# Performance work log

Hardware: AMD Instinct MI355X
Metric: run time of the kernel (lower is better)

The kernel has to match this reference:

```python
import jax, jax.numpy as jnp
import numpy as np

D_MODEL = 768
N_HEADS = 12
HEAD_DIM = D_MODEL // N_HEADS


def setup_inputs() -> dict:
    key = jax.random.key(0)
    ks = jax.random.split(key, 9)
    B, S = 2, 2048
    x = jax.random.normal(ks[0], (B, S, D_MODEL), dtype=jnp.float32)
    s = 1.0 / np.sqrt(D_MODEL)
    Wq = jax.random.normal(ks[1], (D_MODEL, D_MODEL), dtype=jnp.float32) * s
    bq = jax.random.normal(ks[2], (D_MODEL,), dtype=jnp.float32) * 0.01
    Wk = jax.random.normal(ks[3], (D_MODEL, D_MODEL), dtype=jnp.float32) * s
    bk = jax.random.normal(ks[4], (D_MODEL,), dtype=jnp.float32) * 0.01
    Wv = jax.random.normal(ks[5], (D_MODEL, D_MODEL), dtype=jnp.float32) * s
    bv = jax.random.normal(ks[6], (D_MODEL,), dtype=jnp.float32) * 0.01
    Wo = jax.random.normal(ks[7], (D_MODEL, D_MODEL), dtype=jnp.float32) * s
    bo = jax.random.normal(ks[8], (D_MODEL,), dtype=jnp.float32) * 0.01
    return {"x": x, "Wq": Wq, "bq": bq, "Wk": Wk, "bk": bk,
            "Wv": Wv, "bv": bv, "Wo": Wo, "bo": bo}


def reference(x, Wq, bq, Wk, bk, Wv, bv, Wo, bo):
    B, S, _ = x.shape
    H, Dh = N_HEADS, HEAD_DIM
    # Projections (torch Linear: x @ W.T + b; here W stored as [in, out])
    q = (x @ Wq + bq).reshape(B, S, H, Dh)
    k = (x @ Wk + bk).reshape(B, S, H, Dh)
    v = (x @ Wv + bv).reshape(B, S, H, Dh)
    scale = 1.0 / jnp.sqrt(jnp.float32(Dh))
    # NOTE: source applies no causal mask despite the class name.
    scores = jnp.einsum('bqhd,bkhd->bhqk', q, k) * scale
    attn = jax.nn.softmax(scores, axis=-1)
    out = jnp.einsum('bhqk,bkhd->bqhd', attn, v).reshape(B, S, H * Dh)
    return out @ Wo + bo
```

## Files before the change

### kernel.cpp

```cpp
#include <hip/hip_runtime.h>

typedef unsigned short u16;
typedef __fp16 halfx2 __attribute__((ext_vector_type(2)));
typedef __fp16 halfx8 __attribute__((ext_vector_type(8)));
typedef float floatx4 __attribute__((ext_vector_type(4)));
typedef unsigned short u16x4 __attribute__((ext_vector_type(4)));
typedef unsigned short u16x8 __attribute__((ext_vector_type(8)));

#define D_MODEL 768
#define NH 12
#define DH 64
#define SEQ 2048
#define BATCH 2
#define MTOK 4096
#define DQKV 2304

__device__ __forceinline__ u16 f2h(float f) {
    __fp16 h = (__fp16)f;
    return __builtin_bit_cast(u16, h);
}

__device__ __forceinline__ void gload_lds16(const void* g, void* l) {
    __builtin_amdgcn_global_load_lds(
        (const __attribute__((address_space(1))) void*)g,
        (__attribute__((address_space(3))) void*)l, 16, 0, 0);
}


__global__ __launch_bounds__(256) void wprep_kernel(const float* __restrict__ Wq, const float* __restrict__ Wk,
                                                    const float* __restrict__ Wv, const float* __restrict__ Wo,
                                                    const float* __restrict__ x,
                                                    u16* __restrict__ WqkvT, u16* __restrict__ WoT,
                                                    u16* __restrict__ xh) {
    __shared__ u16 t[64][72];
    int bid = blockIdx.x;
    int tid = threadIdx.x;
    if (bid >= 576) {
        int idx = (bid - 576) * 2048 + tid * 8;
        float4 v0 = *(const float4*)(x + idx);
        float4 v1 = *(const float4*)(x + idx + 4);
        union { u16x8 u; halfx2 h[4]; } pk;
        pk.h[0] = __builtin_amdgcn_cvt_pkrtz(v0.x, v0.y);
        pk.h[1] = __builtin_amdgcn_cvt_pkrtz(v0.z, v0.w);
        pk.h[2] = __builtin_amdgcn_cvt_pkrtz(v1.x, v1.y);
        pk.h[3] = __builtin_amdgcn_cvt_pkrtz(v1.z, v1.w);
        *(u16x8*)(xh + idx) = pk.u;
        return;
    }
    int z = bid / 144;
    int t2 = bid % 144;
    int k0 = (t2 / 12) * 64, n0 = (t2 % 12) * 64;
    const float* W = (z == 0) ? Wq : (z == 1) ? Wk : (z == 2) ? Wv : Wo;
    u16* dst = (z < 3) ? (WqkvT + (size_t)z * 768 * 768) : WoT;
#pragma unroll
    for (int p = 0; p < 16; ++p) {
        int idx = p * 256 + tid;
        int kr = idx >> 6, nc = idx & 63;
        t[kr][nc] = f2h(W[(size_t)(k0 + kr) * 768 + n0 + nc]);
    }
    __syncthreads();
#pragma unroll
    for (int p = 0; p < 16; ++p) {
        int idx = p * 256 + tid;
        int nr = idx >> 6, kc = idx & 63;
        dst[(size_t)(n0 + nr) * 768 + k0 + kc] = t[kc][nr];
    }
}


__global__ __launch_bounds__(256) void gemm_qkv(const u16* __restrict__ xh, const u16* __restrict__ Bt,
                                                const float* __restrict__ bq, const float* __restrict__ bk,
                                                const float* __restrict__ bv,
                                                u16* __restrict__ qP, u16* __restrict__ kP,
                                                u16* __restrict__ vTout) {
    const int tid = threadIdx.x;
    const int wid = tid >> 6;
    const int lane = tid & 63;
    const int qd = lane >> 4;
    const int l15 = lane & 15;

    const int tn = blockIdx.x * 128;
    const int tm = blockIdx.y * 64;
    const int wm = (wid >> 1) * 32;
    const int wn = (wid & 1) * 64;

    __shared__ alignas(16) u16 As[64 * 64];
    __shared__ alignas(16) u16 Bs[128 * 64];

    floatx4 acc[2][4];
#pragma unroll
    for (int i = 0; i < 2; ++i)
#pragma unroll
        for (int j = 0; j < 4; ++j) acc[i][j] = (floatx4)(0.0f);

    const u16* Ag[2];
#pragma unroll
    for (int rd = 0; rd < 2; ++rd) {
        int s = rd * 256 + tid;
        int r = s >> 3, bl = (s & 7) ^ (r & 7);
        Ag[rd] = xh + (size_t)(tm + r) * 768 + bl * 8;
    }
    const u16* Bg[4];
#pragma unroll
    for (int rd = 0; rd < 4; ++rd) {
        int s = rd * 256 + tid;
        int r = s >> 3, bl = (s & 7) ^ (r & 7);
        Bg[rd] = Bt + (size_t)(tn + r) * 768 + bl * 8;
    }

    for (int kb = 0; kb < 768; kb += 64) {
        __syncthreads();
#pragma unroll
        for (int rd = 0; rd < 2; ++rd)
            gload_lds16(Ag[rd] + kb, As + (size_t)(rd * 256 + tid) * 8);
#pragma unroll
        for (int rd = 0; rd < 4; ++rd)
            gload_lds16(Bg[rd] + kb, Bs + (size_t)(rd * 256 + tid) * 8);
        __syncthreads();

#pragma unroll
        for (int ks = 0; ks < 2; ++ks) {
            halfx8 af[2], bf[4];
#pragma unroll
            for (int i = 0; i < 2; ++i) {
                int r = wm + i * 16 + l15;
                af[i] = *(const halfx8*)(As + r * 64 + (((ks * 4 + qd) ^ (r & 7)) * 8));
            }
#pragma unroll
            for (int j = 0; j < 4; ++j) {
                int r2 = wn + j * 16 + l15;
                bf[j] = *(const halfx8*)(Bs + r2 * 64 + (((ks * 4 + qd) ^ (r2 & 7)) * 8));
            }
#pragma unroll
            for (int i = 0; i < 2; ++i)
#pragma unroll
                for (int j = 0; j < 4; ++j)
                    acc[i][j] = __builtin_amdgcn_mfma_f32_16x16x32_f16(af[i], bf[j], acc[i][j], 0, 0, 0);
        }
    }

    const float cscale = 0.125f * 1.44269504088896340736f;
    const int rgn = (tn < 768) ? 0 : (tn < 1536) ? 1 : 2;
    const float* bsrc = (rgn == 0) ? bq : (rgn == 1) ? bk : bv;
#pragma unroll
    for (int j = 0; j < 4; ++j) {
        int col = tn + wn + j * 16 + l15;
        int cl = col - rgn * 768;
        float bvv = bsrc[cl];
        int h = cl >> 6, d = cl & 63;
#pragma unroll
        for (int i = 0; i < 2; ++i) {
            int row0 = tm + wm + i * 16 + qd * 4;
            int b = row0 >> 11, s0 = row0 & 2047;
            u16x4 pk;
#pragma unroll
            for (int r = 0; r < 4; ++r) {
                float v = acc[i][j][r] + bvv;
                if (rgn == 0) v *= cscale;
                pk[r] = f2h(v);
            }
            if (rgn == 2) {
                *(u16x4*)(vTout + ((size_t)(b * NH + h) * 64 + d) * SEQ + s0) = pk;
            } else {
                u16* dst = (rgn == 0) ? qP : kP;
#pragma unroll
                for (int r = 0; r < 4; ++r)
                    dst[((size_t)(b * NH + h) * SEQ + s0 + r) * DH + d] = pk[r];
            }
        }
    }
}


__global__ __launch_bounds__(256, 3) void attn_kernel(const u16* __restrict__ qP, const u16* __restrict__ kP,
                                                      const u16* __restrict__ vT, u16* __restrict__ attn) {
    const int tid = threadIdx.x;
    const int wid = tid >> 6;
    const int lane = tid & 63;
    const int qd = lane >> 4;
    const int l15 = lane & 15;

    const int bh = blockIdx.x;
    const int b = bh / NH, h = bh % NH;
    const int q0 = blockIdx.y * 64;

    __shared__ alignas(16) u16 smem[13312];
    u16* qlds = smem;
    u16* ps = smem + 4096 + wid * 2304;

#pragma unroll
    for (int ks = 0; ks < 2; ++ks) {
        halfx8 qv = *(const halfx8*)(qP + (size_t)(bh * SEQ + q0 + wid * 16 + l15) * DH + ks * 32 + qd * 8);
        *(halfx8*)(qlds + (size_t)((ks * 4 + wid) * 64 + lane) * 8) = qv;
    }
    __syncthreads();

    auto AQ = [&](int jn, int ks) -> halfx8 {
        return *(const halfx8*)(qlds + (size_t)((ks * 4 + jn) * 64 + lane) * 8);
    };

    floatx4 o[4][4];
#pragma unroll
    for (int ip = 0; ip < 4; ++ip)
#pragma unroll
        for (int jn = 0; jn < 4; ++jn) o[ip][jn] = (floatx4)(0.0f);
    float lsum[4] = {0.0f, 0.0f, 0.0f, 0.0f};

    const u16* kbase = kP + (size_t)(bh * SEQ + wid * 32 + l15) * DH + qd * 8;
    const u16* vbase = vT + (size_t)(bh * 64 + l15) * SEQ + wid * 32 + qd * 8;

    floatx4 sc[2][4];
    {
        halfx8 ak0[2][2];
#pragma unroll
        for (int mi = 0; mi < 2; ++mi)
#pragma unroll
            for (int ks = 0; ks < 2; ++ks)
                ak0[mi][ks] = *(const halfx8*)(kbase + (size_t)(mi * 16) * DH + ks * 32);
#pragma unroll
        for (int jn = 0; jn < 4; ++jn) {
            halfx8 a0 = AQ(jn, 0), a1 = AQ(jn, 1);
#pragma unroll
            for (int mi = 0; mi < 2; ++mi) {
                floatx4 z = (floatx4)(0.0f);
                z = __builtin_amdgcn_mfma_f32_16x16x32_f16(ak0[mi][0], a0, z, 0, 0, 0);
                sc[mi][jn] = __builtin_amdgcn_mfma_f32_16x16x32_f16(ak0[mi][1], a1, z, 0, 0, 0);
            }
        }
    }

    for (int kt = 0; kt < 16; ++kt) {
        const int kt1 = (kt + 1) & 15;

        halfx8 akn[2][2];
#pragma unroll
        for (int mi = 0; mi < 2; ++mi)
#pragma unroll
            for (int ks = 0; ks < 2; ++ks)
                akn[mi][ks] = *(const halfx8*)(kbase + (size_t)(kt1 * 128 + mi * 16) * DH + ks * 32);
        halfx8 avc[4];
#pragma unroll
        for (int ip = 0; ip < 4; ++ip)
            avc[ip] = *(const halfx8*)(vbase + (size_t)(ip * 16) * SEQ + kt * 128);

#pragma unroll
        for (int mi = 0; mi < 2; ++mi)
#pragma unroll
            for (int jn = 0; jn < 4; ++jn) {
                float p0 = __builtin_amdgcn_exp2f(sc[mi][jn][0]);
                float p1 = __builtin_amdgcn_exp2f(sc[mi][jn][1]);
                float p2 = __builtin_amdgcn_exp2f(sc[mi][jn][2]);
                float p3 = __builtin_amdgcn_exp2f(sc[mi][jn][3]);
                lsum[jn] += (p0 + p1) + (p2 + p3);
                union { u16x4 u; halfx2 h[2]; } pk;
                pk.h[0] = __builtin_amdgcn_cvt_pkrtz(p0, p1);
                pk.h[1] = __builtin_amdgcn_cvt_pkrtz(p2, p3);
                *(u16x4*)(ps + (jn * 16 + l15) * 36 + mi * 16 + qd * 4) = pk.u;
            }

        __builtin_amdgcn_s_setprio(1);
#pragma unroll
        for (int jn = 0; jn < 4; ++jn) {
            halfx8 a0 = AQ(jn, 0), a1 = AQ(jn, 1);
#pragma unroll
            for (int mi = 0; mi < 2; ++mi) {
                floatx4 z = (floatx4)(0.0f);
                z = __builtin_amdgcn_mfma_f32_16x16x32_f16(akn[mi][0], a0, z, 0, 0, 0);
                sc[mi][jn] = __builtin_amdgcn_mfma_f32_16x16x32_f16(akn[mi][1], a1, z, 0, 0, 0);
            }
        }
        __builtin_amdgcn_s_setprio(0);

#pragma unroll
        for (int jn = 0; jn < 4; ++jn) {
            union { halfx8 h8; u16x4 u4[2]; } bpu;
            bpu.u4[0] = *(const u16x4*)(ps + (jn * 16 + l15) * 36 + qd * 8);
            bpu.u4[1] = *(const u16x4*)(ps + (jn * 16 + l15) * 36 + qd * 8 + 4);
            __builtin_amdgcn_s_setprio(1);
#pragma unroll
            for (int ip = 0; ip < 4; ++ip)
                o[ip][jn] = __builtin_amdgcn_mfma_f32_16x16x32_f16(avc[ip], bpu.h8, o[ip][jn], 0, 0, 0);
            __builtin_amdgcn_s_setprio(0);
        }
    }

#pragma unroll
    for (int jn = 0; jn < 4; ++jn) {
        float v = lsum[jn];
        v += __shfl_xor(v, 16, 64);
        v += __shfl_xor(v, 32, 64);
        lsum[jn] = v;
    }

    float* Oacc = (float*)smem;
    float* la = (float*)smem + 4352;

    __syncthreads();
    if (wid == 0) {
#pragma unroll
        for (int jn = 0; jn < 4; ++jn) {
            int q = jn * 16 + l15;
#pragma unroll
            for (int ip = 0; ip < 4; ++ip)
                *(floatx4*)(Oacc + q * 68 + ip * 16 + qd * 4) = o[ip][jn];
            if (qd == 0) la[q] = lsum[jn];
        }
    }
    for (int w = 1; w < 4; ++w) {
        __syncthreads();
        if (wid == w) {
#pragma unroll
            for (int jn = 0; jn < 4; ++jn) {
                int q = jn * 16 + l15;
#pragma unroll
                for (int ip = 0; ip < 4; ++ip) {
                    float* p = Oacc + q * 68 + ip * 16 + qd * 4;
                    *(floatx4*)p = *(floatx4*)p + o[ip][jn];
                }
                if (qd == 0) la[q] += lsum[jn];
            }
        }
    }
    __syncthreads();

    {
        int q = tid >> 2, d0 = (tid & 3) * 16;
        float inv = __builtin_amdgcn_rcpf(la[q]);
        const float* op = Oacc + q * 68 + d0;
        u16x8 pk0, pk1;
#pragma unroll
        for (int r = 0; r < 8; ++r) pk0[r] = f2h(op[r] * inv);
#pragma unroll
        for (int r = 0; r < 8; ++r) pk1[r] = f2h(op[8 + r] * inv);
        u16* dst = attn + (size_t)(b * SEQ + q0 + q) * D_MODEL + h * DH + d0;
        *(u16x8*)dst = pk0;
        *(u16x8*)(dst + 8) = pk1;
    }
}


__global__ __launch_bounds__(256) void gemm_out(const u16* __restrict__ A, const u16* __restrict__ Bt,
                                                const float* __restrict__ bias, float* __restrict__ Cout) {
    const int tid = threadIdx.x;
    const int wid = tid >> 6;
    const int lane = tid & 63;
    const int qd = lane >> 4;
    const int l15 = lane & 15;

    const int tn = blockIdx.x * 64;
    const int tm = blockIdx.y * 64;
    const int wm = (wid >> 1) * 32;
    const int wn = (wid & 1) * 32;

    __shared__ alignas(16) u16 As[64 * 64];
    __shared__ alignas(16) u16 Bs[64 * 64];

    floatx4 acc[2][2];
#pragma unroll
    for (int i = 0; i < 2; ++i)
#pragma unroll
        for (int j = 0; j < 2; ++j) acc[i][j] = (floatx4)(0.0f);

    const u16* Ag[2];
    const u16* Bg[2];
#pragma unroll
    for (int rd = 0; rd < 2; ++rd) {
        int s = rd * 256 + tid;
        int r = s >> 3, bl = (s & 7) ^ (r & 7);
        Ag[rd] = A + (size_t)(tm + r) * 768 + bl * 8;
        Bg[rd] = Bt + (size_t)(tn + r) * 768 + bl * 8;
    }

    for (int kb = 0; kb < 768; kb += 64) {
        __syncthreads();
#pragma unroll
        for (int rd = 0; rd < 2; ++rd) {
            gload_lds16(Ag[rd] + kb, As + (size_t)(rd * 256 + tid) * 8);
            gload_lds16(Bg[rd] + kb, Bs + (size_t)(rd * 256 + tid) * 8);
        }
        __syncthreads();

#pragma unroll
        for (int ks = 0; ks < 2; ++ks) {
            halfx8 af[2], bf[2];
#pragma unroll
            for (int i = 0; i < 2; ++i) {
                int r = wm + i * 16 + l15;
                af[i] = *(const halfx8*)(As + r * 64 + (((ks * 4 + qd) ^ (r & 7)) * 8));
                int r2 = wn + i * 16 + l15;
                bf[i] = *(const halfx8*)(Bs + r2 * 64 + (((ks * 4 + qd) ^ (r2 & 7)) * 8));
            }
#pragma unroll
            for (int i = 0; i < 2; ++i)
#pragma unroll
                for (int j = 0; j < 2; ++j)
                    acc[i][j] = __builtin_amdgcn_mfma_f32_16x16x32_f16(af[i], bf[j], acc[i][j], 0, 0, 0);
        }
    }

#pragma unroll
    for (int j = 0; j < 2; ++j) {
        int col = tn + wn + j * 16 + l15;
        float bv = bias[col];
#pragma unroll
        for (int i = 0; i < 2; ++i) {
            int row0 = tm + wm + i * 16 + qd * 4;
#pragma unroll
            for (int r = 0; r < 4; ++r)
                Cout[(size_t)(row0 + r) * 768 + col] = acc[i][j][r] + bv;
        }
    }
}


extern "C" void kernel_launch(void* const* d_in, const int* in_sizes, int n_in,
                              void* d_out, int out_size, void* d_ws, size_t ws_size,
                              hipStream_t stream) {
    const float* x  = (const float*)d_in[0];
    const float* Wq = (const float*)d_in[1];
    const float* bq = (const float*)d_in[2];
    const float* Wk = (const float*)d_in[3];
    const float* bk = (const float*)d_in[4];
    const float* Wv = (const float*)d_in[5];
    const float* bv = (const float*)d_in[6];
    const float* Wo = (const float*)d_in[7];
    const float* bo = (const float*)d_in[8];

    char* ws = (char*)d_ws;
    size_t off = 0;
    auto take = [&](size_t bytes) -> char* {
        char* p = ws + off;
        off += (bytes + 255) & ~(size_t)255;
        return p;
    };
    u16* WqkvT = (u16*)take((size_t)DQKV * D_MODEL * 2);
    u16* WoT   = (u16*)take((size_t)D_MODEL * D_MODEL * 2);
    u16* qP    = (u16*)take((size_t)MTOK * D_MODEL * 2);
    u16* kP    = (u16*)take((size_t)MTOK * D_MODEL * 2);
    u16* vTb   = (u16*)take((size_t)BATCH * NH * DH * SEQ * 2);
    u16* attn  = (u16*)take((size_t)MTOK * D_MODEL * 2);
    u16* xh = attn;

    wprep_kernel<<<576 + (MTOK * D_MODEL / 2048), 256, 0, stream>>>(Wq, Wk, Wv, Wo, x, WqkvT, WoT, xh);
    gemm_qkv<<<dim3(DQKV / 128, MTOK / 64), 256, 0, stream>>>(xh, WqkvT, bq, bk, bv, qP, kP, vTb);
    attn_kernel<<<dim3(BATCH * NH, SEQ / 64), 256, 0, stream>>>(qP, kP, vTb, attn);
    gemm_out<<<dim3(D_MODEL / 64, MTOK / 64), 256, 0, stream>>>(attn, WoT, bo, (float*)d_out);
}
```

Baseline: 197.5 us.

## Split PV output across waves by head-dim with shared P tile

Each wave now owns 16 head-dim columns of the output instead of a partial sum over its own key slice. P tiles from all waves go into a double-buffered shared array and are read by every wave after a per-iteration barrier. This removes the serialized cross-wave reduction of 64x64 fp32 accumulators at the end and shrinks the output accumulator registers fourfold. Q fragments are also kept in registers instead of reloaded from LDS. The cost is a __syncthreads inside every key-tile iteration and a larger shared P buffer.

New measurement: 185.2 us. 1.07x faster.

```diff
diff --git a/kernel.cpp b/kernel.cpp
--- a/kernel.cpp
+++ b/kernel.cpp
@@ -184,30 +184,22 @@
     const int b = bh / NH, h = bh % NH;
     const int q0 = blockIdx.y * 64;
 
-    __shared__ alignas(16) u16 smem[13312];
-    u16* qlds = smem;
-    u16* ps = smem + 4096 + wid * 2304;
-
-#pragma unroll
-    for (int ks = 0; ks < 2; ++ks) {
-        halfx8 qv = *(const halfx8*)(qP + (size_t)(bh * SEQ + q0 + wid * 16 + l15) * DH + ks * 32 + qd * 8);
-        *(halfx8*)(qlds + (size_t)((ks * 4 + wid) * 64 + lane) * 8) = qv;
-    }
-    __syncthreads();
-
-    auto AQ = [&](int jn, int ks) -> halfx8 {
-        return *(const halfx8*)(qlds + (size_t)((ks * 4 + jn) * 64 + lane) * 8);
-    };
-
-    floatx4 o[4][4];
-#pragma unroll
-    for (int ip = 0; ip < 4; ++ip)
-#pragma unroll
-        for (int jn = 0; jn < 4; ++jn) o[ip][jn] = (floatx4)(0.0f);
+    __shared__ alignas(16) u16 smem[2 * 64 * 136];
+
+    halfx8 aq[4][2];
+#pragma unroll
+    for (int jn = 0; jn < 4; ++jn)
+#pragma unroll
+        for (int ks = 0; ks < 2; ++ks)
+            aq[jn][ks] = *(const halfx8*)(qP + (size_t)(bh * SEQ + q0 + jn * 16 + l15) * DH + ks * 32 + qd * 8);
+
+    floatx4 o[4];
+#pragma unroll
+    for (int jn = 0; jn < 4; ++jn) o[jn] = (floatx4)(0.0f);
     float lsum[4] = {0.0f, 0.0f, 0.0f, 0.0f};
 
     const u16* kbase = kP + (size_t)(bh * SEQ + wid * 32 + l15) * DH + qd * 8;
-    const u16* vbase = vT + (size_t)(bh * 64 + l15) * SEQ + wid * 32 + qd * 8;
+    const u16* vbase = vT + (size_t)(bh * 64 + wid * 16 + l15) * SEQ + qd * 8;
 
     floatx4 sc[2][4];
     {
@@ -219,17 +211,17 @@
                 ak0[mi][ks] = *(const halfx8*)(kbase + (size_t)(mi * 16) * DH + ks * 32);
 #pragma unroll
         for (int jn = 0; jn < 4; ++jn) {
-            halfx8 a0 = AQ(jn, 0), a1 = AQ(jn, 1);
 #pragma unroll
             for (int mi = 0; mi < 2; ++mi) {
                 floatx4 z = (floatx4)(0.0f);
-                z = __builtin_amdgcn_mfma_f32_16x16x32_f16(ak0[mi][0], a0, z, 0, 0, 0);
-                sc[mi][jn] = __builtin_amdgcn_mfma_f32_16x16x32_f16(ak0[mi][1], a1, z, 0, 0, 0);
+                z = __builtin_amdgcn_mfma_f32_16x16x32_f16(ak0[mi][0], aq[jn][0], z, 0, 0, 0);
+                sc[mi][jn] = __builtin_amdgcn_mfma_f32_16x16x32_f16(ak0[mi][1], aq[jn][1], z, 0, 0, 0);
             }
         }
     }
 
     for (int kt = 0; kt < 16; ++kt) {
+        u16* pbuf = smem + (size_t)(kt & 1) * (64 * 136);
         const int kt1 = (kt + 1) & 15;
 
         halfx8 akn[2][2];
@@ -240,8 +232,8 @@
                 akn[mi][ks] = *(const halfx8*)(kbase + (size_t)(kt1 * 128 + mi * 16) * DH + ks * 32);
         halfx8 avc[4];
 #pragma unroll
-        for (int ip = 0; ip < 4; ++ip)
-            avc[ip] = *(const halfx8*)(vbase + (size_t)(ip * 16) * SEQ + kt * 128);
+        for (int ks = 0; ks < 4; ++ks)
+            avc[ks] = *(const halfx8*)(vbase + kt * 128 + ks * 32);
 
 #pragma unroll
         for (int mi = 0; mi < 2; ++mi)
@@ -255,33 +247,33 @@
                 union { u16x4 u; halfx2 h[2]; } pk;
                 pk.h[0] = __builtin_amdgcn_cvt_pkrtz(p0, p1);
                 pk.h[1] = __builtin_amdgcn_cvt_pkrtz(p2, p3);
-                *(u16x4*)(ps + (jn * 16 + l15) * 36 + mi * 16 + qd * 4) = pk.u;
+                *(u16x4*)(pbuf + (jn * 16 + l15) * 136 + wid * 32 + mi * 16 + qd * 4) = pk.u;
             }
 
         __builtin_amdgcn_s_setprio(1);
 #pragma unroll
         for (int jn = 0; jn < 4; ++jn) {
-            halfx8 a0 = AQ(jn, 0), a1 = AQ(jn, 1);
 #pragma unroll
             for (int mi = 0; mi < 2; ++mi) {
                 floatx4 z = (floatx4)(0.0f);
-                z = __builtin_amdgcn_mfma_f32_16x16x32_f16(akn[mi][0], a0, z, 0, 0, 0);
-                sc[mi][jn] = __builtin_amdgcn_mfma_f32_16x16x32_f16(akn[mi][1], a1, z, 0, 0, 0);
+                z = __builtin_amdgcn_mfma_f32_16x16x32_f16(akn[mi][0], aq[jn][0], z, 0, 0, 0);
+                sc[mi][jn] = __builtin_amdgcn_mfma_f32_16x16x32_f16(akn[mi][1], aq[jn][1], z, 0, 0, 0);
             }
         }
         __builtin_amdgcn_s_setprio(0);
 
-#pragma unroll
-        for (int jn = 0; jn < 4; ++jn) {
-            union { halfx8 h8; u16x4 u4[2]; } bpu;
-            bpu.u4[0] = *(const u16x4*)(ps + (jn * 16 + l15) * 36 + qd * 8);
-            bpu.u4[1] = *(const u16x4*)(ps + (jn * 16 + l15) * 36 + qd * 8 + 4);
-            __builtin_amdgcn_s_setprio(1);
-#pragma unroll
-            for (int ip = 0; ip < 4; ++ip)
-                o[ip][jn] = __builtin_amdgcn_mfma_f32_16x16x32_f16(avc[ip], bpu.h8, o[ip][jn], 0, 0, 0);
-            __builtin_amdgcn_s_setprio(0);
-        }
+        __syncthreads();
+
+        __builtin_amdgcn_s_setprio(1);
+#pragma unroll
+        for (int ks = 0; ks < 4; ++ks) {
+#pragma unroll
+            for (int jn = 0; jn < 4; ++jn) {
+                halfx8 bp = *(const halfx8*)(pbuf + (jn * 16 + l15) * 136 + ks * 32 + qd * 8);
+                o[jn] = __builtin_amdgcn_mfma_f32_16x16x32_f16(avc[ks], bp, o[jn], 0, 0, 0);
+            }
+        }
+        __builtin_amdgcn_s_setprio(0);
     }
 
 #pragma unroll
@@ -292,49 +284,24 @@
         lsum[jn] = v;
     }
 
-    float* Oacc = (float*)smem;
-    float* la = (float*)smem + 4352;
-
+    float* la4 = (float*)smem;
+    if (qd == 0) {
+#pragma unroll
+        for (int jn = 0; jn < 4; ++jn)
+            la4[wid * 64 + jn * 16 + l15] = lsum[jn];
+    }
     __syncthreads();
-    if (wid == 0) {
-#pragma unroll
-        for (int jn = 0; jn < 4; ++jn) {
-            int q = jn * 16 + l15;
-#pragma unroll
-            for (int ip = 0; ip < 4; ++ip)
-                *(floatx4*)(Oacc + q * 68 + ip * 16 + qd * 4) = o[ip][jn];
-            if (qd == 0) la[q] = lsum[jn];
-        }
-    }
-    for (int w = 1; w < 4; ++w) {
-        __syncthreads();
-        if (wid == w) {
-#pragma unroll
-            for (int jn = 0; jn < 4; ++jn) {
-                int q = jn * 16 + l15;
-#pragma unroll
-                for (int ip = 0; ip < 4; ++ip) {
-                    float* p = Oacc + q * 68 + ip * 16 + qd * 4;
-                    *(floatx4*)p = *(floatx4*)p + o[ip][jn];
-                }
-                if (qd == 0) la[q] += lsum[jn];
-            }
-        }
-    }
-    __syncthreads();
-
-    {
-        int q = tid >> 2, d0 = (tid & 3) * 16;
-        float inv = __builtin_amdgcn_rcpf(la[q]);
-        const float* op = Oacc + q * 68 + d0;
-        u16x8 pk0, pk1;
-#pragma unroll
-        for (int r = 0; r < 8; ++r) pk0[r] = f2h(op[r] * inv);
-#pragma unroll
-        for (int r = 0; r < 8; ++r) pk1[r] = f2h(op[8 + r] * inv);
-        u16* dst = attn + (size_t)(b * SEQ + q0 + q) * D_MODEL + h * DH + d0;
-        *(u16x8*)dst = pk0;
-        *(u16x8*)(dst + 8) = pk1;
+
+#pragma unroll
+    for (int jn = 0; jn < 4; ++jn) {
+        int q = jn * 16 + l15;
+        float s = (la4[q] + la4[64 + q]) + (la4[128 + q] + la4[192 + q]);
+        float inv = __builtin_amdgcn_rcpf(s);
+        u16x4 pk;
+#pragma unroll
+        for (int r = 0; r < 4; ++r) pk[r] = f2h(o[jn][r] * inv);
+        u16* dst = attn + (size_t)(b * SEQ + q0 + q) * D_MODEL + h * DH + wid * 16 + qd * 4;
+        *(u16x4*)dst = pk;
     }
 }
 
```

## Software-pipeline attention loop with double-buffered P tiles and register-resident Q

Applied to the files above, without the earlier changes.

Restructures the attention main loop into a deeper software pipeline. K tiles are prefetched two iterations ahead, V is double-buffered in registers, and the softmax probability tile is double-buffered in LDS so the QK, exp and PV stages of different iterations overlap. Q fragments are now held in registers instead of being staged through LDS, which removes the initial barrier. The extra register and LDS use lowers the occupancy hint from 3 to 2 blocks per CU, which may reduce latency hiding.

Measured after the change: 206.6 us. 1.05x slower.

```diff
diff --git a/kernel.cpp b/kernel.cpp
--- a/kernel.cpp
+++ b/kernel.cpp
@@ -172,7 +172,7 @@
 }
 
 
-__global__ __launch_bounds__(256, 3) void attn_kernel(const u16* __restrict__ qP, const u16* __restrict__ kP,
+__global__ __launch_bounds__(256, 2) void attn_kernel(const u16* __restrict__ qP, const u16* __restrict__ kP,
                                                       const u16* __restrict__ vT, u16* __restrict__ attn) {
     const int tid = threadIdx.x;
     const int wid = tid >> 6;
@@ -184,20 +184,16 @@
     const int b = bh / NH, h = bh % NH;
     const int q0 = blockIdx.y * 64;
 
-    __shared__ alignas(16) u16 smem[13312];
-    u16* qlds = smem;
-    u16* ps = smem + 4096 + wid * 2304;
-
-#pragma unroll
-    for (int ks = 0; ks < 2; ++ks) {
-        halfx8 qv = *(const halfx8*)(qP + (size_t)(bh * SEQ + q0 + wid * 16 + l15) * DH + ks * 32 + qd * 8);
-        *(halfx8*)(qlds + (size_t)((ks * 4 + wid) * 64 + lane) * 8) = qv;
-    }
-    __syncthreads();
-
-    auto AQ = [&](int jn, int ks) -> halfx8 {
-        return *(const halfx8*)(qlds + (size_t)((ks * 4 + jn) * 64 + lane) * 8);
-    };
+    __shared__ alignas(16) u16 smem[18432];
+    u16* ps0 = smem + wid * 4608;
+    u16* ps1 = ps0 + 2304;
+
+    halfx8 aq[4][2];
+#pragma unroll
+    for (int jn = 0; jn < 4; ++jn)
+#pragma unroll
+        for (int ks = 0; ks < 2; ++ks)
+            aq[jn][ks] = *(const halfx8*)(qP + (size_t)(bh * SEQ + q0 + jn * 16 + l15) * DH + ks * 32 + qd * 8);
 
     floatx4 o[4][4];
 #pragma unroll
@@ -209,40 +205,10 @@
     const u16* kbase = kP + (size_t)(bh * SEQ + wid * 32 + l15) * DH + qd * 8;
     const u16* vbase = vT + (size_t)(bh * 64 + l15) * SEQ + wid * 32 + qd * 8;
 
+    halfx8 kA[2][2], kB[2][2], vA[4], vB[4];
     floatx4 sc[2][4];
-    {
-        halfx8 ak0[2][2];
-#pragma unroll
-        for (int mi = 0; mi < 2; ++mi)
-#pragma unroll
-            for (int ks = 0; ks < 2; ++ks)
-                ak0[mi][ks] = *(const halfx8*)(kbase + (size_t)(mi * 16) * DH + ks * 32);
-#pragma unroll
-        for (int jn = 0; jn < 4; ++jn) {
-            halfx8 a0 = AQ(jn, 0), a1 = AQ(jn, 1);
-#pragma unroll
-            for (int mi = 0; mi < 2; ++mi) {
-                floatx4 z = (floatx4)(0.0f);
-                z = __builtin_amdgcn_mfma_f32_16x16x32_f16(ak0[mi][0], a0, z, 0, 0, 0);
-                sc[mi][jn] = __builtin_amdgcn_mfma_f32_16x16x32_f16(ak0[mi][1], a1, z, 0, 0, 0);
-            }
-        }
-    }
-
-    for (int kt = 0; kt < 16; ++kt) {
-        const int kt1 = (kt + 1) & 15;
-
-        halfx8 akn[2][2];
-#pragma unroll
-        for (int mi = 0; mi < 2; ++mi)
-#pragma unroll
-            for (int ks = 0; ks < 2; ++ks)
-                akn[mi][ks] = *(const halfx8*)(kbase + (size_t)(kt1 * 128 + mi * 16) * DH + ks * 32);
-        halfx8 avc[4];
-#pragma unroll
-        for (int ip = 0; ip < 4; ++ip)
-            avc[ip] = *(const halfx8*)(vbase + (size_t)(ip * 16) * SEQ + kt * 128);
-
+
+    auto expstore = [&](u16* buf) {
 #pragma unroll
         for (int mi = 0; mi < 2; ++mi)
 #pragma unroll
@@ -255,34 +221,72 @@
                 union { u16x4 u; halfx2 h[2]; } pk;
                 pk.h[0] = __builtin_amdgcn_cvt_pkrtz(p0, p1);
                 pk.h[1] = __builtin_amdgcn_cvt_pkrtz(p2, p3);
-                *(u16x4*)(ps + (jn * 16 + l15) * 36 + mi * 16 + qd * 4) = pk.u;
-            }
-
+                *(u16x4*)(buf + (jn * 16 + l15) * 36 + mi * 16 + qd * 4) = pk.u;
+            }
+    };
+    auto qk = [&](halfx8 (&ak)[2][2]) {
         __builtin_amdgcn_s_setprio(1);
 #pragma unroll
         for (int jn = 0; jn < 4; ++jn) {
-            halfx8 a0 = AQ(jn, 0), a1 = AQ(jn, 1);
 #pragma unroll
             for (int mi = 0; mi < 2; ++mi) {
                 floatx4 z = (floatx4)(0.0f);
-                z = __builtin_amdgcn_mfma_f32_16x16x32_f16(akn[mi][0], a0, z, 0, 0, 0);
-                sc[mi][jn] = __builtin_amdgcn_mfma_f32_16x16x32_f16(akn[mi][1], a1, z, 0, 0, 0);
+                z = __builtin_amdgcn_mfma_f32_16x16x32_f16(ak[mi][0], aq[jn][0], z, 0, 0, 0);
+                sc[mi][jn] = __builtin_amdgcn_mfma_f32_16x16x32_f16(ak[mi][1], aq[jn][1], z, 0, 0, 0);
             }
         }
         __builtin_amdgcn_s_setprio(0);
-
+    };
+    auto pv = [&](const u16* buf, halfx8 (&av)[4]) {
 #pragma unroll
         for (int jn = 0; jn < 4; ++jn) {
             union { halfx8 h8; u16x4 u4[2]; } bpu;
-            bpu.u4[0] = *(const u16x4*)(ps + (jn * 16 + l15) * 36 + qd * 8);
-            bpu.u4[1] = *(const u16x4*)(ps + (jn * 16 + l15) * 36 + qd * 8 + 4);
+            bpu.u4[0] = *(const u16x4*)(buf + (jn * 16 + l15) * 36 + qd * 8);
+            bpu.u4[1] = *(const u16x4*)(buf + (jn * 16 + l15) * 36 + qd * 8 + 4);
             __builtin_amdgcn_s_setprio(1);
 #pragma unroll
             for (int ip = 0; ip < 4; ++ip)
-                o[ip][jn] = __builtin_amdgcn_mfma_f32_16x16x32_f16(avc[ip], bpu.h8, o[ip][jn], 0, 0, 0);
+                o[ip][jn] = __builtin_amdgcn_mfma_f32_16x16x32_f16(av[ip], bpu.h8, o[ip][jn], 0, 0, 0);
             __builtin_amdgcn_s_setprio(0);
         }
-    }
+    };
+    auto loadK = [&](halfx8 (&dst)[2][2], int t) {
+#pragma unroll
+        for (int mi = 0; mi < 2; ++mi)
+#pragma unroll
+            for (int ks = 0; ks < 2; ++ks)
+                dst[mi][ks] = *(const halfx8*)(kbase + (size_t)(((t)&15) * 128 + mi * 16) * DH + ks * 32);
+    };
+    auto loadV = [&](halfx8 (&dst)[4], int t) {
+#pragma unroll
+        for (int ip = 0; ip < 4; ++ip)
+            dst[ip] = *(const halfx8*)(vbase + (size_t)(ip * 16) * SEQ + ((t)&15) * 128);
+    };
+
+    loadK(kA, 0);
+    loadK(kB, 1);
+    qk(kA);
+    loadK(kA, 2);
+    loadV(vA, 0);
+    expstore(ps0);
+    qk(kB);
+
+    auto body = [&](int t, u16* bufW, u16* bufR,
+                    halfx8 (&kO)[2][2], halfx8 (&kN)[2][2],
+                    halfx8 (&vO)[4], halfx8 (&vN)[4]) {
+        if (t < 14) loadK(kN, t + 2);
+        loadV(vN, t);
+        expstore(bufW);
+        if (t < 15) qk(kO);
+        pv(bufR, vO);
+    };
+
+    body(1, ps1, ps0, kA, kB, vA, vB);
+    for (int t = 2; t < 16; t += 2) {
+        body(t,     ps0, ps1, kB, kA, vB, vA);
+        body(t + 1, ps1, ps0, kA, kB, vA, vB);
+    }
+    pv(ps1, vB);
 
 #pragma unroll
     for (int jn = 0; jn < 4; ++jn) {
```
